# Optimization experiments

Measured on AMD Instinct MI355X. Metric: run time of the kernel, lower is better.

## Reference

```python
import jax, jax.numpy as jnp
import numpy as np

DIM = 512
HEADS = 8
DIM_HEAD = 64
INNER = HEADS * DIM_HEAD  # 512
BN_EPS = 1e-5


def _bn(x, gamma, beta, mean, var):
    # BatchNorm1d in eval mode over channel axis 1 of [b, c, n]
    inv = gamma / jnp.sqrt(var + BN_EPS)
    return x * inv[None, :, None] + (beta - mean * inv)[None, :, None]


def setup_inputs() -> dict:
    key = jax.random.key(0)
    ks = jax.random.split(key, 12)
    b, d, n = 4, DIM, 2048
    s = 0.02
    return {
        "x": jax.random.normal(ks[0], (b, d, n), dtype=jnp.float32),
        "W_qkv": jax.random.normal(ks[1], (3 * INNER, DIM), dtype=jnp.float32) * s,
        "W_out": jax.random.normal(ks[2], (DIM, INNER), dtype=jnp.float32) * s,
        "b_out": jax.random.normal(ks[3], (DIM,), dtype=jnp.float32) * s,
        "g1": jax.random.normal(ks[4], (DIM,), dtype=jnp.float32) * 0.1 + 1.0,
        "beta1": jax.random.normal(ks[5], (DIM,), dtype=jnp.float32) * 0.1,
        "m1": jax.random.normal(ks[6], (DIM,), dtype=jnp.float32) * 0.1,
        "v1": jax.random.uniform(ks[7], (DIM,), minval=0.5, maxval=1.5, dtype=jnp.float32),
        "W_ffn": jax.random.normal(ks[8], (DIM, DIM), dtype=jnp.float32) * s,
        "g2": jax.random.normal(ks[9], (DIM,), dtype=jnp.float32) * 0.1 + 1.0,
        "beta2": jax.random.normal(ks[10], (DIM,), dtype=jnp.float32) * 0.1,
        "m2": jax.random.normal(ks[11], (DIM,), dtype=jnp.float32) * 0.1,
        "v2": jax.random.uniform(jax.random.fold_in(key, 99), (DIM,), minval=0.5, maxval=1.5, dtype=jnp.float32),
    }


def reference(x, W_qkv, W_out, b_out, g1, beta1, m1, v1, W_ffn, g2, beta2, m2, v2):
    b, d, n = x.shape
    h, dh = HEADS, DIM_HEAD
    scale = dh ** -0.5

    # ---- Attention (manual QKV + einsum softmax attention) ----
    xt = jnp.einsum("bdn->bnd", x)                       # [b, n, d]
    qkv = xt @ W_qkv.T                                   # [b, n, 3*inner]
    q, k, v = jnp.split(qkv, 3, axis=-1)
    def to_heads(t):
        return t.reshape(b, n, h, dh).transpose(0, 2, 1, 3)  # [b, h, n, dh]
    q, k, v = to_heads(q), to_heads(k), to_heads(v)
    dots = jnp.einsum("bhid,bhjd->bhij", q, k) * scale   # [b, h, n, n]
    attn = jax.nn.softmax(dots, axis=-1)
    out = jnp.einsum("bhij,bhjd->bhid", attn, v)         # [b, h, n, dh]
    out = out.transpose(0, 2, 1, 3).reshape(b, n, h * dh).transpose(0, 2, 1)  # [b, inner, n]
    # to_out: Conv1d(inner, dim, 1, bias=True) + BatchNorm1d(dim)
    out = jnp.einsum("oc,bcn->bon", W_out, out) + b_out[None, :, None]
    att_out = _bn(out, g1, beta1, m1, v1)

    # ---- Residual + GELU, then FFN (Conv1d 1x1 no bias + BN), residual + GELU ----
    att = jax.nn.gelu(att_out + x, approximate=False)
    ffn = _bn(jnp.einsum("oc,bcn->bon", W_ffn, att), g2, beta2, m2, v2)
    return jax.nn.gelu(att + ffn, approximate=False)
```

## Files before the change

### kernel.cpp

```cpp
#include <hip/hip_runtime.h>
#include <math.h>

#define N_TOK 2048

typedef __attribute__((ext_vector_type(8))) short short8;
typedef __attribute__((ext_vector_type(4))) float f32x4;

__device__ __forceinline__ float gelu_f(float v) {
    return 0.5f * v * (1.0f + erff(v * 0.7071067811865475f));
}
__device__ __forceinline__ ushort f2bf(float x) {
    uint u = __float_as_uint(x);
    uint r = u + 0x7FFFu + ((u >> 16) & 1u);
    return (ushort)(r >> 16);
}
__device__ __forceinline__ float bf2f(ushort u) {
    return __uint_as_float((uint)u << 16);
}
__device__ __forceinline__ void gload16(const void* g, void* s) {
    __builtin_amdgcn_global_load_lds((const __attribute__((address_space(1))) void*)g,
                                     (__attribute__((address_space(3))) void*)s, 16, 0, 0);
}

__global__ __launch_bounds__(256)
void prep(const float* __restrict__ w0, ushort* __restrict__ o0,
          const float* __restrict__ w1, ushort* __restrict__ o1,
          const float* __restrict__ w2, ushort* __restrict__ o2,
          const float* __restrict__ x, ushort* __restrict__ xt)
{
    __shared__ ushort sT[64 * 68];
    const int tid = threadIdx.x;
    int bx = blockIdx.x;
    if (bx < 1280) {
        int i4 = bx * 256 + tid;
        const float* src; ushort* dst; int idx;
        if (i4 < 196608)      { src = w0; dst = o0; idx = i4; }
        else if (i4 < 262144) { src = w1; dst = o1; idx = i4 - 196608; }
        else                  { src = w2; dst = o2; idx = i4 - 262144; }
        float4 v = *(const float4*)&src[idx * 4];
        ushort4 p; p.x = f2bf(v.x); p.y = f2bf(v.y); p.z = f2bf(v.z); p.w = f2bf(v.w);
        *(ushort4*)&dst[idx * 4] = p;
        return;
    }
    bx -= 1280;
    const int tok0 = (bx & 31) * 64;
    const int ch0 = ((bx >> 5) & 7) * 64;
    const int bi = bx >> 8;
    #pragma unroll
    for (int i = 0; i < 4; i++) {
        int ch = (tid >> 4) + i * 16;
        int t4 = (tid & 15) * 4;
        float4 v = *(const float4*)&x[((size_t)bi * 512 + ch0 + ch) * N_TOK + tok0 + t4];
        ushort4 p; p.x = f2bf(v.x); p.y = f2bf(v.y); p.z = f2bf(v.z); p.w = f2bf(v.w);
        *(ushort4*)&sT[ch * 68 + t4] = p;
    }
    __syncthreads();
    const int tr = (tid & 15) + (tid >> 6) * 16;
    const int cb = ((tid >> 4) & 3) * 16;
    uint vv[8];
    #pragma unroll
    for (int j = 0; j < 8; j++) {
        uint lo = sT[(cb + 2 * j) * 68 + tr];
        uint hi = sT[(cb + 2 * j + 1) * 68 + tr];
        vv[j] = lo | (hi << 16);
    }
    size_t base = ((size_t)bi * N_TOK + tok0 + tr) * 512 + ch0 + cb;
    *(uint4*)&xt[base]     = *(uint4*)&vv[0];
    *(uint4*)&xt[base + 8] = *(uint4*)&vv[4];
}

template<int MODE, int BM, int BN>
__global__ __launch_bounds__(256)
void bgemm(const ushort* __restrict__ A, const ushort* __restrict__ Bt, int M,
           ushort* __restrict__ qt, ushort* __restrict__ vc,
           float* __restrict__ outF, ushort* __restrict__ outB,
           const float* __restrict__ bias,
           const float* __restrict__ g, const float* __restrict__ be,
           const float* __restrict__ mu, const float* __restrict__ va,
           const ushort* __restrict__ residB)
{
    constexpr int MF = BM / 32, NF = BN / 32;
    __shared__ ushort sA[BM * 64];
    __shared__ ushort sB[BN * 64];
    const int tid = threadIdx.x;
    const int w = tid >> 6, l = tid & 63;
    const int l16 = l & 15, lg = l >> 4;
    const int wr = w >> 1, wc = w & 1;
    const int bi = blockIdx.z;
    const int m0 = blockIdx.y * BM, n0 = blockIdx.x * BN;
    const ushort* Bb = Bt + (size_t)bi * N_TOK * 512;
    const int srow = l >> 3, spos = l & 7;

    f32x4 acc[MF][NF];
    #pragma unroll
    for (int i = 0; i < MF; i++)
        #pragma unroll
        for (int j = 0; j < NF; j++) acc[i][j] = (f32x4){0.f, 0.f, 0.f, 0.f};

    for (int kt = 0; kt < 512; kt += 64) {
        __syncthreads();
        #pragma unroll
        for (int i = 0; i < BM / 32; i++) {
            int row = w * (BM / 4) + i * 8 + srow;
            int c = spos ^ (row & 7);
            gload16(A + (size_t)(m0 + row) * 512 + kt + c * 8,
                    sA + (w * (BM / 4) + i * 8) * 64);
        }
        #pragma unroll
        for (int i = 0; i < BN / 32; i++) {
            int row = w * (BN / 4) + i * 8 + srow;
            int c = spos ^ (row & 7);
            gload16(Bb + (size_t)(n0 + row) * 512 + kt + c * 8,
                    sB + (w * (BN / 4) + i * 8) * 64);
        }
        __syncthreads();
        #pragma unroll
        for (int ks = 0; ks < 2; ks++) {
            short8 af[MF], bfv[NF];
            #pragma unroll
            for (int mi = 0; mi < MF; mi++) {
                int row = wr * (BM / 2) + mi * 16 + l16;
                af[mi] = *(const short8*)&sA[row * 64 + (((ks * 4 + lg) ^ (row & 7)) << 3)];
            }
            #pragma unroll
            for (int ni = 0; ni < NF; ni++) {
                int row = wc * (BN / 2) + ni * 16 + l16;
                bfv[ni] = *(const short8*)&sB[row * 64 + (((ks * 4 + lg) ^ (row & 7)) << 3)];
            }
            __builtin_amdgcn_s_setprio(1);
            #pragma unroll
            for (int mi = 0; mi < MF; mi++)
                #pragma unroll
                for (int ni = 0; ni < NF; ni++)
                    acc[mi][ni] = __builtin_amdgcn_mfma_f32_16x16x32_bf16(
                        af[mi], bfv[ni], acc[mi][ni], 0, 0, 0);
            __builtin_amdgcn_s_setprio(0);
        }
    }

    const int chb = m0 + wr * (BM / 2);
    const int tkb = n0 + wc * (BN / 2);
    if (MODE == 0) {
        if (m0 < 1024) {
            const float qs = (m0 < 512) ? 0.18033688f : 1.0f;
            #pragma unroll
            for (int mi = 0; mi < MF; mi++) {
                int ob = chb + mi * 16 + lg * 4;
                #pragma unroll
                for (int ni = 0; ni < NF; ni++) {
                    int tok = tkb + ni * 16 + l16;
                    ushort4 p;
                    p.x = f2bf(acc[mi][ni][0] * qs); p.y = f2bf(acc[mi][ni][1] * qs);
                    p.z = f2bf(acc[mi][ni][2] * qs); p.w = f2bf(acc[mi][ni][3] * qs);
                    *(ushort4*)&qt[((size_t)bi * N_TOK + tok) * 1024 + ob] = p;
                }
            }
        } else {
            #pragma unroll
            for (int mi = 0; mi < MF; mi++)
                #pragma unroll
                for (int r = 0; r < 4; r++) {
                    int o = chb + mi * 16 + lg * 4 + r - 1024;
                    #pragma unroll
                    for (int ni = 0; ni < NF; ni++) {
                        int tok = tkb + ni * 16 + l16;
                        vc[((size_t)bi * 512 + o) * N_TOK + tok] = f2bf(acc[mi][ni][r]);
                    }
                }
        }
    } else {
        #pragma unroll
        for (int mi = 0; mi < MF; mi++) {
            float inv[4], sh[4], bb[4];
            #pragma unroll
            for (int r = 0; r < 4; r++) {
                int o = chb + mi * 16 + lg * 4 + r;
                inv[r] = g[o] * rsqrtf(va[o] + 1e-5f);
                sh[r]  = be[o] - mu[o] * inv[r];
                bb[r]  = (MODE == 1) ? bias[o] : 0.f;
            }
            #pragma unroll
            for (int ni = 0; ni < NF; ni++) {
                int tok = tkb + ni * 16 + l16;
                ushort4 rv = *(const ushort4*)&residB[((size_t)bi * N_TOK + tok) * 512 +
                                                      chb + mi * 16 + lg * 4];
                float rr_[4] = {bf2f(rv.x), bf2f(rv.y), bf2f(rv.z), bf2f(rv.w)};
                float ov[4];
                #pragma unroll
                for (int r = 0; r < 4; r++) {
                    float y = (acc[mi][ni][r] + bb[r]) * inv[r] + sh[r];
                    ov[r] = gelu_f((MODE == 1) ? (y + rr_[r]) : (rr_[r] + y));
                }
                if (MODE == 1) {
                    ushort4 p;
                    p.x = f2bf(ov[0]); p.y = f2bf(ov[1]);
                    p.z = f2bf(ov[2]); p.w = f2bf(ov[3]);
                    *(ushort4*)&outB[((size_t)bi * N_TOK + tok) * 512 +
                                     chb + mi * 16 + lg * 4] = p;
                } else {
                    #pragma unroll
                    for (int r = 0; r < 4; r++) {
                        int o = chb + mi * 16 + lg * 4 + r;
                        outF[((size_t)bi * 512 + o) * N_TOK + tok] = ov[r];
                    }
                }
            }
        }
    }
}

__global__ __launch_bounds__(256)
void attn_mfma(const ushort* __restrict__ qt, const ushort* __restrict__ vc,
               ushort* __restrict__ aout)
{
    __shared__ ushort sK[2][64 * 64];
    __shared__ ushort sV[2][64 * 64];
    __shared__ uint   sPu[4][512];
    const int tid = threadIdx.x;
    const int w = tid >> 6, l = tid & 63;
    const int l16 = l & 15, lg = l >> 4;
    const int h = blockIdx.y, bi = blockIdx.z;
    const int qw = blockIdx.x * 64 + w * 16;
    const int srow = l >> 3, spos = l & 7;
    const int swz = (l16 & 7) << 2;
    uint* sPw = &sPu[w][0];

    const ushort* kSrc = qt + (size_t)bi * N_TOK * 1024 + 512 + h * 64 + ((spos ^ srow) << 3);
    const ushort* vSrc = vc + (size_t)(bi * 512 + h * 64) * N_TOK + ((spos ^ srow) << 3);

    short8 qf[2];
    #pragma unroll
    for (int kt = 0; kt < 2; kt++)
        qf[kt] = *(const short8*)(qt +
            ((size_t)(bi * N_TOK + qw + l16) * 1024 + h * 64 + kt * 32 + lg * 8));

    f32x4 oacc[4];
    #pragma unroll
    for (int dt = 0; dt < 4; dt++) oacc[dt] = (f32x4){0.f, 0.f, 0.f, 0.f};
    float lsum = 0.f;

    #pragma unroll
    for (int i = 0; i < 2; i++) {
        int rk = w * 16 + i * 8;
        gload16(kSrc + (size_t)(rk + srow) * 1024, &sK[0][rk * 64]);
        gload16(vSrc + (size_t)(rk + srow) * N_TOK, &sV[0][rk * 64]);
    }

    for (int t = 0; t < N_TOK / 64; t++) {
        const int cur = t & 1;
        __syncthreads();
        if (t + 1 < N_TOK / 64) {
            const int kv1 = (t + 1) * 64;
            #pragma unroll
            for (int i = 0; i < 2; i++) {
                int rk = w * 16 + i * 8;
                gload16(kSrc + (size_t)(kv1 + rk + srow) * 1024, &sK[cur ^ 1][rk * 64]);
                gload16(vSrc + (size_t)(rk + srow) * N_TOK + kv1, &sV[cur ^ 1][rk * 64]);
            }
        }

        f32x4 sacc[4];
        #pragma unroll
        for (int nt = 0; nt < 4; nt++) sacc[nt] = (f32x4){0.f, 0.f, 0.f, 0.f};
        __builtin_amdgcn_s_setprio(1);
        #pragma unroll
        for (int nt = 0; nt < 4; nt++)
            #pragma unroll
            for (int kt = 0; kt < 2; kt++) {
                short8 kf = *(const short8*)&sK[cur][(nt * 16 + l16) * 64 +
                                                     (((kt * 4 + lg) ^ (l16 & 7)) << 3)];
                sacc[nt] = __builtin_amdgcn_mfma_f32_16x16x32_bf16(
                    kf, qf[kt], sacc[nt], 0, 0, 0);
            }
        __builtin_amdgcn_s_setprio(0);

        float ps = 0.f;
        #pragma unroll
        for (int nt = 0; nt < 4; nt++)
            #pragma unroll
            for (int r = 0; r < 4; r++) {
                float p = __builtin_amdgcn_exp2f(sacc[nt][r]);
                sacc[nt][r] = p;
                ps += p;
            }
        ps += __shfl_xor(ps, 16);
        ps += __shfl_xor(ps, 32);
        lsum += ps;

        #pragma unroll
        for (int nt = 0; nt < 4; nt++) {
            float a0 = sacc[nt][0], a1 = sacc[nt][1], a2 = sacc[nt][2], a3 = sacc[nt][3];
            uint u0, u1;
            asm("v_cvt_pk_bf16_f32 %0, %1, %2" : "=v"(u0) : "v"(a0), "v"(a1));
            asm("v_cvt_pk_bf16_f32 %0, %1, %2" : "=v"(u1) : "v"(a2), "v"(a3));
            int col = ((nt * 4 + lg) * 2) ^ swz;
            *(uint2*)&sPw[l16 * 32 + col] = make_uint2(u0, u1);
        }

        #pragma unroll
        for (int kt = 0; kt < 2; kt++) {
            short8 pf = *(const short8*)&sPw[l16 * 32 + ((kt * 16 + lg * 4) ^ swz)];
            __builtin_amdgcn_s_setprio(1);
            #pragma unroll
            for (int dt = 0; dt < 4; dt++) {
                short8 vf = *(const short8*)&sV[cur][(dt * 16 + l16) * 64 +
                                                     (((kt * 4 + lg) ^ (l16 & 7)) << 3)];
                oacc[dt] = __builtin_amdgcn_mfma_f32_16x16x32_bf16(
                    pf, vf, oacc[dt], 0, 0, 0);
            }
            __builtin_amdgcn_s_setprio(0);
        }
    }

    float rl = 1.f / lsum;
    float rr[4];
    #pragma unroll
    for (int r = 0; r < 4; r++) rr[r] = __shfl(rl, lg * 4 + r);
    #pragma unroll
    for (int dt = 0; dt < 4; dt++) {
        int ch = h * 64 + dt * 16 + l16;
        #pragma unroll
        for (int r = 0; r < 4; r++) {
            int tok = qw + lg * 4 + r;
            aout[((size_t)bi * N_TOK + tok) * 512 + ch] = f2bf(oacc[dt][r] * rr[r]);
        }
    }
}

extern "C" void kernel_launch(void* const* d_in, const int* in_sizes, int n_in,
                              void* d_out, int out_size, void* d_ws, size_t ws_size,
                              hipStream_t stream) {
    const float* x    = (const float*)d_in[0];
    const float* Wqkv = (const float*)d_in[1];
    const float* Wout = (const float*)d_in[2];
    const float* bout = (const float*)d_in[3];
    const float* g1   = (const float*)d_in[4];
    const float* be1  = (const float*)d_in[5];
    const float* m1   = (const float*)d_in[6];
    const float* v1   = (const float*)d_in[7];
    const float* Wffn = (const float*)d_in[8];
    const float* g2   = (const float*)d_in[9];
    const float* be2  = (const float*)d_in[10];
    const float* m2   = (const float*)d_in[11];
    const float* v2   = (const float*)d_in[12];

    char* ws = (char*)d_ws;
    ushort* wqB  = (ushort*)(ws + 0);
    ushort* woB  = (ushort*)(ws + 1572864);
    ushort* wfB  = (ushort*)(ws + 2097152);
    ushort* xt   = (ushort*)(ws + 2621440);
    ushort* qtp  = (ushort*)(ws + 11010048);
    ushort* vcp  = (ushort*)(ws + 27787264);
    ushort* aout = (ushort*)(ws + 36175872);
    ushort* attB = (ushort*)(ws + 27787264);

    dim3 blk(256);
    prep<<<2304, blk, 0, stream>>>(Wqkv, wqB, Wout, woB, Wffn, wfB, x, xt);
    bgemm<0, 128, 128><<<dim3(16, 12, 4), blk, 0, stream>>>(
        wqB, xt, 1536, qtp, vcp, nullptr, nullptr,
        nullptr, nullptr, nullptr, nullptr, nullptr, nullptr);
    attn_mfma<<<dim3(32, 8, 4), blk, 0, stream>>>(qtp, vcp, aout);
    bgemm<1, 64, 128><<<dim3(16, 8, 4), blk, 0, stream>>>(
        woB, aout, 512, nullptr, nullptr, nullptr, attB,
        bout, g1, be1, m1, v1, xt);
    bgemm<2, 64, 128><<<dim3(16, 8, 4), blk, 0, stream>>>(
        wfB, attB, 512, nullptr, nullptr, (float*)d_out, nullptr,
        nullptr, g2, be2, m2, v2, attB);
}
```

Before: 123.5 us.

## Process two query tiles per wave in attention to reuse K/V fragments

Each wave in the attention kernel now handles 32 query rows (two 16-row M-tiles) instead of 16. Every K and V fragment read from LDS feeds two MFMAs, and the block covers 128 queries, so the grid is halved. This cuts LDS fragment reads and global K/V reloads per query. In exchange it roughly doubles accumulator registers, enlarges the P scratch buffer, and leaves 512 blocks instead of 1024, which may lower occupancy.

```diff
diff --git a/kernel.cpp b/kernel.cpp
--- a/kernel.cpp
+++ b/kernel.cpp
@@ -215,12 +215,12 @@
 {
     __shared__ ushort sK[2][64 * 64];
     __shared__ ushort sV[2][64 * 64];
-    __shared__ uint   sPu[4][512];
+    __shared__ uint   sPu[4][1024];
     const int tid = threadIdx.x;
     const int w = tid >> 6, l = tid & 63;
     const int l16 = l & 15, lg = l >> 4;
     const int h = blockIdx.y, bi = blockIdx.z;
-    const int qw = blockIdx.x * 64 + w * 16;
+    const int qw = blockIdx.x * 128 + w * 32;
     const int srow = l >> 3, spos = l & 7;
     const int swz = (l16 & 7) << 2;
     uint* sPw = &sPu[w][0];
@@ -228,16 +228,20 @@
     const ushort* kSrc = qt + (size_t)bi * N_TOK * 1024 + 512 + h * 64 + ((spos ^ srow) << 3);
     const ushort* vSrc = vc + (size_t)(bi * 512 + h * 64) * N_TOK + ((spos ^ srow) << 3);
 
-    short8 qf[2];
-    #pragma unroll
-    for (int kt = 0; kt < 2; kt++)
-        qf[kt] = *(const short8*)(qt +
-            ((size_t)(bi * N_TOK + qw + l16) * 1024 + h * 64 + kt * 32 + lg * 8));
-
-    f32x4 oacc[4];
-    #pragma unroll
-    for (int dt = 0; dt < 4; dt++) oacc[dt] = (f32x4){0.f, 0.f, 0.f, 0.f};
-    float lsum = 0.f;
+    short8 qf[2][2];
+    #pragma unroll
+    for (int Mt = 0; Mt < 2; Mt++)
+        #pragma unroll
+        for (int kt = 0; kt < 2; kt++)
+            qf[Mt][kt] = *(const short8*)(qt +
+                ((size_t)(bi * N_TOK + qw + Mt * 16 + l16) * 1024 + h * 64 + kt * 32 + lg * 8));
+
+    f32x4 oacc[2][4];
+    #pragma unroll
+    for (int Mt = 0; Mt < 2; Mt++)
+        #pragma unroll
+        for (int dt = 0; dt < 4; dt++) oacc[Mt][dt] = (f32x4){0.f, 0.f, 0.f, 0.f};
+    float lsum[2] = {0.f, 0.f};
 
     #pragma unroll
     for (int i = 0; i < 2; i++) {
@@ -259,9 +263,11 @@
             }
         }
 
-        f32x4 sacc[4];
-        #pragma unroll
-        for (int nt = 0; nt < 4; nt++) sacc[nt] = (f32x4){0.f, 0.f, 0.f, 0.f};
+        f32x4 sacc[2][4];
+        #pragma unroll
+        for (int Mt = 0; Mt < 2; Mt++)
+            #pragma unroll
+            for (int nt = 0; nt < 4; nt++) sacc[Mt][nt] = (f32x4){0.f, 0.f, 0.f, 0.f};
         __builtin_amdgcn_s_setprio(1);
         #pragma unroll
         for (int nt = 0; nt < 4; nt++)
@@ -269,60 +275,74 @@
             for (int kt = 0; kt < 2; kt++) {
                 short8 kf = *(const short8*)&sK[cur][(nt * 16 + l16) * 64 +
                                                      (((kt * 4 + lg) ^ (l16 & 7)) << 3)];
-                sacc[nt] = __builtin_amdgcn_mfma_f32_16x16x32_bf16(
-                    kf, qf[kt], sacc[nt], 0, 0, 0);
+                #pragma unroll
+                for (int Mt = 0; Mt < 2; Mt++)
+                    sacc[Mt][nt] = __builtin_amdgcn_mfma_f32_16x16x32_bf16(
+                        kf, qf[Mt][kt], sacc[Mt][nt], 0, 0, 0);
             }
         __builtin_amdgcn_s_setprio(0);
 
-        float ps = 0.f;
-        #pragma unroll
-        for (int nt = 0; nt < 4; nt++)
-            #pragma unroll
-            for (int r = 0; r < 4; r++) {
-                float p = __builtin_amdgcn_exp2f(sacc[nt][r]);
-                sacc[nt][r] = p;
-                ps += p;
-            }
-        ps += __shfl_xor(ps, 16);
-        ps += __shfl_xor(ps, 32);
-        lsum += ps;
-
-        #pragma unroll
-        for (int nt = 0; nt < 4; nt++) {
-            float a0 = sacc[nt][0], a1 = sacc[nt][1], a2 = sacc[nt][2], a3 = sacc[nt][3];
-            uint u0, u1;
-            asm("v_cvt_pk_bf16_f32 %0, %1, %2" : "=v"(u0) : "v"(a0), "v"(a1));
-            asm("v_cvt_pk_bf16_f32 %0, %1, %2" : "=v"(u1) : "v"(a2), "v"(a3));
-            int col = ((nt * 4 + lg) * 2) ^ swz;
-            *(uint2*)&sPw[l16 * 32 + col] = make_uint2(u0, u1);
+        #pragma unroll
+        for (int Mt = 0; Mt < 2; Mt++) {
+            float ps = 0.f;
+            #pragma unroll
+            for (int nt = 0; nt < 4; nt++)
+                #pragma unroll
+                for (int r = 0; r < 4; r++) {
+                    float p = __builtin_amdgcn_exp2f(sacc[Mt][nt][r]);
+                    sacc[Mt][nt][r] = p;
+                    ps += p;
+                }
+            ps += __shfl_xor(ps, 16);
+            ps += __shfl_xor(ps, 32);
+            lsum[Mt] += ps;
+            #pragma unroll
+            for (int nt = 0; nt < 4; nt++) {
+                float a0 = sacc[Mt][nt][0], a1 = sacc[Mt][nt][1];
+                float a2 = sacc[Mt][nt][2], a3 = sacc[Mt][nt][3];
+                uint u0, u1;
+                asm("v_cvt_pk_bf16_f32 %0, %1, %2" : "=v"(u0) : "v"(a0), "v"(a1));
+                asm("v_cvt_pk_bf16_f32 %0, %1, %2" : "=v"(u1) : "v"(a2), "v"(a3));
+                int col = ((nt * 4 + lg) * 2) ^ swz;
+                *(uint2*)&sPw[Mt * 512 + l16 * 32 + col] = make_uint2(u0, u1);
+            }
         }
 
         #pragma unroll
         for (int kt = 0; kt < 2; kt++) {
-            short8 pf = *(const short8*)&sPw[l16 * 32 + ((kt * 16 + lg * 4) ^ swz)];
+            short8 pf[2];
+            #pragma unroll
+            for (int Mt = 0; Mt < 2; Mt++)
+                pf[Mt] = *(const short8*)&sPw[Mt * 512 + l16 * 32 +
+                                              ((kt * 16 + lg * 4) ^ swz)];
             __builtin_amdgcn_s_setprio(1);
             #pragma unroll
             for (int dt = 0; dt < 4; dt++) {
                 short8 vf = *(const short8*)&sV[cur][(dt * 16 + l16) * 64 +
                                                      (((kt * 4 + lg) ^ (l16 & 7)) << 3)];
-                oacc[dt] = __builtin_amdgcn_mfma_f32_16x16x32_bf16(
-                    pf, vf, oacc[dt], 0, 0, 0);
+                #pragma unroll
+                for (int Mt = 0; Mt < 2; Mt++)
+                    oacc[Mt][dt] = __builtin_amdgcn_mfma_f32_16x16x32_bf16(
+                        pf[Mt], vf, oacc[Mt][dt], 0, 0, 0);
             }
             __builtin_amdgcn_s_setprio(0);
         }
     }
 
-    float rl = 1.f / lsum;
-    float rr[4];
-    #pragma unroll
-    for (int r = 0; r < 4; r++) rr[r] = __shfl(rl, lg * 4 + r);
-    #pragma unroll
-    for (int dt = 0; dt < 4; dt++) {
-        int ch = h * 64 + dt * 16 + l16;
-        #pragma unroll
-        for (int r = 0; r < 4; r++) {
-            int tok = qw + lg * 4 + r;
-            aout[((size_t)bi * N_TOK + tok) * 512 + ch] = f2bf(oacc[dt][r] * rr[r]);
+    #pragma unroll
+    for (int Mt = 0; Mt < 2; Mt++) {
+        float rl = 1.f / lsum[Mt];
+        float rr[4];
+        #pragma unroll
+        for (int r = 0; r < 4; r++) rr[r] = __shfl(rl, lg * 4 + r);
+        #pragma unroll
+        for (int dt = 0; dt < 4; dt++) {
+            int ch = h * 64 + dt * 16 + l16;
+            #pragma unroll
+            for (int r = 0; r < 4; r++) {
+                int tok = qw + Mt * 16 + lg * 4 + r;
+                aout[((size_t)bi * N_TOK + tok) * 512 + ch] = f2bf(oacc[Mt][dt][r] * rr[r]);
+            }
         }
     }
 }
@@ -359,7 +379,7 @@
     bgemm<0, 128, 128><<<dim3(16, 12, 4), blk, 0, stream>>>(
         wqB, xt, 1536, qtp, vcp, nullptr, nullptr,
         nullptr, nullptr, nullptr, nullptr, nullptr, nullptr);
-    attn_mfma<<<dim3(32, 8, 4), blk, 0, stream>>>(qtp, vcp, aout);
+    attn_mfma<<<dim3(16, 8, 4), blk, 0, stream>>>(qtp, vcp, aout);
     bgemm<1, 64, 128><<<dim3(16, 8, 4), blk, 0, stream>>>(
         woB, aout, 512, nullptr, nullptr, nullptr, attB,
         bout, g1, be1, m1, v1, xt);
```

Measured after the change: 122.7 us. No clear change (-0.6%).

## Rewrite attention with 32x32x16 MFMA, register-resident P via permlane swap

Applied to the files above, without the earlier changes.

The attention kernel switches from 16x16x32 to 32x32x16 bf16 MFMA tiles, with each wave handling 32 query rows instead of 16. The probability matrix now stays in registers: v_permlane32_swap rearranges the packed bf16 values into the A-operand layout, so the LDS round trip through sP is gone. Blocks shrink to 2 waves and the grid is flattened to 1D with a remapped block order so that blocks sharing the same head and batch are spread across XCDs. The costs are fewer waves per block, larger accumulator register use, and a different cache locality pattern.

```diff
diff --git a/kernel.cpp b/kernel.cpp
--- a/kernel.cpp
+++ b/kernel.cpp
@@ -5,6 +5,7 @@
 
 typedef __attribute__((ext_vector_type(8))) short short8;
 typedef __attribute__((ext_vector_type(4))) float f32x4;
+typedef __attribute__((ext_vector_type(16))) float f32x16;
 
 __device__ __forceinline__ float gelu_f(float v) {
     return 0.5f * v * (1.0f + erff(v * 0.7071067811865475f));
@@ -209,41 +210,44 @@
     }
 }
 
-__global__ __launch_bounds__(256)
+__global__ __launch_bounds__(128)
 void attn_mfma(const ushort* __restrict__ qt, const ushort* __restrict__ vc,
                ushort* __restrict__ aout)
 {
     __shared__ ushort sK[2][64 * 64];
     __shared__ ushort sV[2][64 * 64];
-    __shared__ uint   sPu[4][512];
     const int tid = threadIdx.x;
     const int w = tid >> 6, l = tid & 63;
-    const int l16 = l & 15, lg = l >> 4;
-    const int h = blockIdx.y, bi = blockIdx.z;
-    const int qw = blockIdx.x * 64 + w * 16;
+    const int c = l & 31, h = l >> 5;
+    const int phys = blockIdx.x;
+    const int logi = (phys & 7) * 128 + (phys >> 3);
+    const int qblk = logi & 31;
+    const int pair = logi >> 5;
+    const int hh = pair & 7, bi = pair >> 3;
+    const int qw = qblk * 64 + w * 32;
     const int srow = l >> 3, spos = l & 7;
-    const int swz = (l16 & 7) << 2;
-    uint* sPw = &sPu[w][0];
-
-    const ushort* kSrc = qt + (size_t)bi * N_TOK * 1024 + 512 + h * 64 + ((spos ^ srow) << 3);
-    const ushort* vSrc = vc + (size_t)(bi * 512 + h * 64) * N_TOK + ((spos ^ srow) << 3);
-
-    short8 qf[2];
-    #pragma unroll
-    for (int kt = 0; kt < 2; kt++)
-        qf[kt] = *(const short8*)(qt +
-            ((size_t)(bi * N_TOK + qw + l16) * 1024 + h * 64 + kt * 32 + lg * 8));
-
-    f32x4 oacc[4];
-    #pragma unroll
-    for (int dt = 0; dt < 4; dt++) oacc[dt] = (f32x4){0.f, 0.f, 0.f, 0.f};
+
+    const ushort* kSrc = qt + (size_t)bi * N_TOK * 1024 + 512 + hh * 64 + ((spos ^ srow) << 3);
+    const ushort* vSrc = vc + (size_t)(bi * 512 + hh * 64) * N_TOK + ((spos ^ srow) << 3);
+
+    short8 qf[4];
+    #pragma unroll
+    for (int dk = 0; dk < 4; dk++)
+        qf[dk] = *(const short8*)(qt +
+            (size_t)(bi * N_TOK + qw + c) * 1024 + hh * 64 + dk * 16 + h * 8);
+
+    f32x16 oacc[2];
+    #pragma unroll
+    for (int dt = 0; dt < 2; dt++)
+        #pragma unroll
+        for (int i = 0; i < 16; i++) oacc[dt][i] = 0.f;
     float lsum = 0.f;
 
     #pragma unroll
-    for (int i = 0; i < 2; i++) {
-        int rk = w * 16 + i * 8;
-        gload16(kSrc + (size_t)(rk + srow) * 1024, &sK[0][rk * 64]);
-        gload16(vSrc + (size_t)(rk + srow) * N_TOK, &sV[0][rk * 64]);
+    for (int i = 0; i < 4; i++) {
+        int rb = i * 16 + w * 8;
+        gload16(kSrc + (size_t)(rb + srow) * 1024, &sK[0][rb * 64]);
+        gload16(vSrc + (size_t)(rb + srow) * N_TOK, &sV[0][rb * 64]);
     }
 
     for (int t = 0; t < N_TOK / 64; t++) {
@@ -252,79 +256,90 @@
         if (t + 1 < N_TOK / 64) {
             const int kv1 = (t + 1) * 64;
             #pragma unroll
-            for (int i = 0; i < 2; i++) {
-                int rk = w * 16 + i * 8;
-                gload16(kSrc + (size_t)(kv1 + rk + srow) * 1024, &sK[cur ^ 1][rk * 64]);
-                gload16(vSrc + (size_t)(rk + srow) * N_TOK + kv1, &sV[cur ^ 1][rk * 64]);
-            }
-        }
-
-        f32x4 sacc[4];
-        #pragma unroll
-        for (int nt = 0; nt < 4; nt++) sacc[nt] = (f32x4){0.f, 0.f, 0.f, 0.f};
-        __builtin_amdgcn_s_setprio(1);
-        #pragma unroll
-        for (int nt = 0; nt < 4; nt++)
-            #pragma unroll
-            for (int kt = 0; kt < 2; kt++) {
-                short8 kf = *(const short8*)&sK[cur][(nt * 16 + l16) * 64 +
-                                                     (((kt * 4 + lg) ^ (l16 & 7)) << 3)];
-                sacc[nt] = __builtin_amdgcn_mfma_f32_16x16x32_bf16(
-                    kf, qf[kt], sacc[nt], 0, 0, 0);
-            }
-        __builtin_amdgcn_s_setprio(0);
-
-        float ps = 0.f;
-        #pragma unroll
-        for (int nt = 0; nt < 4; nt++)
-            #pragma unroll
-            for (int r = 0; r < 4; r++) {
-                float p = __builtin_amdgcn_exp2f(sacc[nt][r]);
-                sacc[nt][r] = p;
-                ps += p;
-            }
-        ps += __shfl_xor(ps, 16);
-        ps += __shfl_xor(ps, 32);
-        lsum += ps;
-
-        #pragma unroll
-        for (int nt = 0; nt < 4; nt++) {
-            float a0 = sacc[nt][0], a1 = sacc[nt][1], a2 = sacc[nt][2], a3 = sacc[nt][3];
-            uint u0, u1;
-            asm("v_cvt_pk_bf16_f32 %0, %1, %2" : "=v"(u0) : "v"(a0), "v"(a1));
-            asm("v_cvt_pk_bf16_f32 %0, %1, %2" : "=v"(u1) : "v"(a2), "v"(a3));
-            int col = ((nt * 4 + lg) * 2) ^ swz;
-            *(uint2*)&sPw[l16 * 32 + col] = make_uint2(u0, u1);
-        }
-
-        #pragma unroll
-        for (int kt = 0; kt < 2; kt++) {
-            short8 pf = *(const short8*)&sPw[l16 * 32 + ((kt * 16 + lg * 4) ^ swz)];
+            for (int i = 0; i < 4; i++) {
+                int rb = i * 16 + w * 8;
+                gload16(kSrc + (size_t)(kv1 + rb + srow) * 1024,
+                        &sK[cur ^ 1][rb * 64]);
+                gload16(vSrc + (size_t)(rb + srow) * N_TOK + kv1,
+                        &sV[cur ^ 1][rb * 64]);
+            }
+        }
+
+        #pragma unroll
+        for (int s = 0; s < 2; s++) {
+            f32x16 sacc;
+            #pragma unroll
+            for (int i = 0; i < 16; i++) sacc[i] = 0.f;
             __builtin_amdgcn_s_setprio(1);
             #pragma unroll
-            for (int dt = 0; dt < 4; dt++) {
-                short8 vf = *(const short8*)&sV[cur][(dt * 16 + l16) * 64 +
-                                                     (((kt * 4 + lg) ^ (l16 & 7)) << 3)];
-                oacc[dt] = __builtin_amdgcn_mfma_f32_16x16x32_bf16(
-                    pf, vf, oacc[dt], 0, 0, 0);
+            for (int dk = 0; dk < 4; dk++) {
+                int row = s * 32 + c;
+                short8 kf = *(const short8*)&sK[cur][row * 64 +
+                             (((dk * 2 + h) ^ (row & 7)) << 3)];
+                sacc = __builtin_amdgcn_mfma_f32_32x32x16_bf16(kf, qf[dk], sacc, 0, 0, 0);
             }
             __builtin_amdgcn_s_setprio(0);
-        }
-    }
-
+
+            uint u0_0, u0_1, u1_0, u1_1, u2_0, u2_1, u3_0, u3_1;
+            float ps = 0.f;
+            {
+                float p0, p1, p2, p3;
+#define PACK_G(G, U0, U1) \
+                p0 = __builtin_amdgcn_exp2f(sacc[4*G+0]); \
+                p1 = __builtin_amdgcn_exp2f(sacc[4*G+1]); \
+                p2 = __builtin_amdgcn_exp2f(sacc[4*G+2]); \
+                p3 = __builtin_amdgcn_exp2f(sacc[4*G+3]); \
+                ps += (p0 + p1) + (p2 + p3); \
+                asm("v_cvt_pk_bf16_f32 %0, %1, %2" : "=v"(U0) : "v"(p0), "v"(p1)); \
+                asm("v_cvt_pk_bf16_f32 %0, %1, %2" : "=v"(U1) : "v"(p2), "v"(p3));
+                PACK_G(0, u0_0, u0_1)
+                PACK_G(1, u1_0, u1_1)
+                PACK_G(2, u2_0, u2_1)
+                PACK_G(3, u3_0, u3_1)
+#undef PACK_G
+            }
+            lsum += ps;
+
+#define PV_STEP(T2, A0, A1, B0, B1) \
+            { \
+                uint a0 = A0, b0 = B0, a1 = A1, b1 = B1; \
+                asm volatile("v_permlane32_swap_b32 %0, %1" : "+v"(b0), "+v"(a0)); \
+                asm volatile("v_permlane32_swap_b32 %0, %1" : "+v"(b1), "+v"(a1)); \
+                uint4 fu = make_uint4(a0, a1, b0, b1); \
+                short8 pf = *(short8*)&fu; \
+                __builtin_amdgcn_s_setprio(1); \
+                _Pragma("unroll") \
+                for (int dt = 0; dt < 2; dt++) { \
+                    int row = dt * 32 + c; \
+                    short8 vf = *(const short8*)&sV[cur][row * 64 + \
+                                 (((s * 4 + T2 * 2 + h) ^ (row & 7)) << 3)]; \
+                    oacc[dt] = __builtin_amdgcn_mfma_f32_32x32x16_bf16( \
+                        pf, vf, oacc[dt], 0, 0, 0); \
+                } \
+                __builtin_amdgcn_s_setprio(0); \
+            }
+            PV_STEP(0, u0_0, u0_1, u1_0, u1_1)
+            PV_STEP(1, u2_0, u2_1, u3_0, u3_1)
+#undef PV_STEP
+        }
+    }
+
+    lsum += __shfl_xor(lsum, 32);
     float rl = 1.f / lsum;
-    float rr[4];
-    #pragma unroll
-    for (int r = 0; r < 4; r++) rr[r] = __shfl(rl, lg * 4 + r);
-    #pragma unroll
-    for (int dt = 0; dt < 4; dt++) {
-        int ch = h * 64 + dt * 16 + l16;
-        #pragma unroll
-        for (int r = 0; r < 4; r++) {
-            int tok = qw + lg * 4 + r;
-            aout[((size_t)bi * N_TOK + tok) * 512 + ch] = f2bf(oacc[dt][r] * rr[r]);
-        }
-    }
+    #pragma unroll
+    for (int dt = 0; dt < 2; dt++)
+        #pragma unroll
+        for (int g = 0; g < 4; g++) {
+            float o0 = oacc[dt][4 * g + 0] * rl;
+            float o1 = oacc[dt][4 * g + 1] * rl;
+            float o2 = oacc[dt][4 * g + 2] * rl;
+            float o3 = oacc[dt][4 * g + 3] * rl;
+            uint p0, p1;
+            asm("v_cvt_pk_bf16_f32 %0, %1, %2" : "=v"(p0) : "v"(o0), "v"(o1));
+            asm("v_cvt_pk_bf16_f32 %0, %1, %2" : "=v"(p1) : "v"(o2), "v"(o3));
+            int ch = hh * 64 + dt * 32 + 8 * g + 4 * h;
+            *(uint2*)&aout[((size_t)bi * N_TOK + qw + c) * 512 + ch] = make_uint2(p0, p1);
+        }
 }
 
 extern "C" void kernel_launch(void* const* d_in, const int* in_sizes, int n_in,
@@ -359,7 +374,7 @@
     bgemm<0, 128, 128><<<dim3(16, 12, 4), blk, 0, stream>>>(
         wqB, xt, 1536, qtp, vcp, nullptr, nullptr,
         nullptr, nullptr, nullptr, nullptr, nullptr, nullptr);
-    attn_mfma<<<dim3(32, 8, 4), blk, 0, stream>>>(qtp, vcp, aout);
+    attn_mfma<<<dim3(1024), dim3(128), 0, stream>>>(qtp, vcp, aout);
     bgemm<1, 64, 128><<<dim3(16, 8, 4), blk, 0, stream>>>(
         woB, aout, 512, nullptr, nullptr, nullptr, attB,
         bout, g1, be1, m1, v1, xt);
```

Result: no change. 123.0 us (-0.4%).
